# Kernel optimization log

Measured on AMD Instinct MI355X. Metric: run time of the kernel, lower is better.

The kernel has to match this reference:

```python
import jax, jax.numpy as jnp
import numpy as np

L_S = 4  # segment length (== factor in __init__)


def dtw_dist(x, y):
    """Exact 1-D DTW distance with |a-b| cost (the quantity fastdtw approximates).

    Row recurrence d[i,j] = C[i,j] + min(d[i-1,j], d[i-1,j-1], d[i,j-1]) is
    solved per row in closed form: with a[j]=min(prev[j],prev[j-1]),
    b[j]=C[i,j]+a[j], S=cumsum(C[i]), we have d[i,:] = S + cummin(b - S).
    """
    C = jnp.abs(x[:, None] - y[None, :])  # [n, m] cost matrix
    big = jnp.asarray(jnp.finfo(C.dtype).max, C.dtype)
    row0 = jnp.cumsum(C[0])  # first DP row: cumulative cost

    def step(prev, c):
        shifted = jnp.concatenate([jnp.full((1,), big, prev.dtype), prev[:-1]])
        a = jnp.minimum(prev, shifted)          # min(d[i-1,j], d[i-1,j-1])
        S = jnp.cumsum(c)
        d = S + jax.lax.cummin(a + c - S)       # min-plus prefix scan
        return d, None

    last, _ = jax.lax.scan(step, row0, C[1:])
    return last[-1]


def setup_inputs() -> dict:
    key = jax.random.key(0)
    kq, kk, kv = jax.random.split(key, 3)
    B, L, H, D = 1, 32, 8, 32
    return {
        "queries": jax.random.normal(kq, (B, L, H, D), dtype=jnp.float32),
        "keys": jax.random.normal(kk, (B, L, H, D), dtype=jnp.float32),
        "values": jax.random.normal(kv, (B, L, H, D), dtype=jnp.float32),
        "attn_mask": jnp.zeros((1,), dtype=bool),  # unused, as in original
    }


def reference(queries, keys, values, attn_mask):
    B, Lq, H, D = queries.shape
    Lk = keys.shape[1]
    Ls = L_S
    scale = 1.0 / np.sqrt(Ls).astype(np.float32)
    Nq, Nk = Lq // Ls, Lk // Ls  # L divisible by Ls -> no addition_Q path

    seg_q = queries.reshape(B, Nq, Ls, H, D)
    seg_k = keys.reshape(B, Nk, Ls, H, D)
    seg_v = values.reshape(B, Nk, Ls, H, D)

    # Original flattens each segment over (B, Ls, H, D) before fastdtw, so the
    # distance is identical for every (b, h): a single [Nq, Nk] matrix.
    flat_q = jnp.moveaxis(seg_q, 1, 0).reshape(Nq, -1)  # [Nq, B*Ls*H*D]
    flat_k = jnp.moveaxis(seg_k, 1, 0).reshape(Nk, -1)  # [Nk, B*Ls*H*D]

    dists = jax.vmap(lambda xq: jax.vmap(lambda xk: dtw_dist(xq, xk))(flat_k))(flat_q)  # [Nq, Nk]

    A = jax.nn.softmax(scale * dists, axis=-1)  # [Nq, Nk], broadcast over (B, H)

    # Softmax-weighted sum of value segments (intended semantics of the
    # expanded matmul): V[b,i,t,h,d] = sum_j A[i,j] * seg_v[b,j,t,h,d]
    V = jnp.einsum('ij,bjthd->bithd', A, seg_v).reshape(B, Nq * Ls, H, D)
    return V
```

## Files before the change

### kernel.cpp

```cpp
#include <hip/hip_runtime.h>
#include <float.h>

#define NSEG 8
#define SEGLEN 1024
#define BIGV 1e30f
#define PADV 1e18f

#define NW 4
#define CH 64
#define NCH 17
#define XLEN 1152
#define BSTRIDE 1160

#define DPPF(OLD, SRC, CTRL, RM, BM, BC)                                      \
    __int_as_float(__builtin_amdgcn_update_dpp(                               \
        __float_as_int(OLD), __float_as_int(SRC), CTRL, RM, BM, BC))
#define WSHIFT1(OLD, SRC) DPPF(OLD, SRC, 0x138, 0xF, 0xF, false)

__device__ __forceinline__ float readlaneF(float v, int l) {
    return __int_as_float(__builtin_amdgcn_readlane(__float_as_int(v), l));
}

__global__ __launch_bounds__(256) void dtw_sk4_kernel(const float* __restrict__ q,
                                                      const float* __restrict__ kk,
                                                      float* __restrict__ dists) {
    __shared__ float xl[XLEN];
    __shared__ float bnd[NW + 1][BSTRIDE];
    __shared__ float dump[128];
    __shared__ int flagsA[NW + 1];
    const int tid = threadIdx.x;
    const int lane = tid & 63;
    const int wv = tid >> 6;
    const int pair = blockIdx.x;
    const float* __restrict__ x = q + (pair >> 3) * SEGLEN;
    const float* __restrict__ y = kk + (pair & 7) * SEGLEN;

    for (int t = tid; t < XLEN; t += 256) xl[t] = (t < SEGLEN) ? x[t] : PADV;
    for (int t = tid; t < (NW + 1) * BSTRIDE; t += 256)
        (&bnd[0][0])[t] = (t == 63) ? 0.f : BIGV;
    if (tid < NW + 1) flagsA[tid] = (tid == 0) ? 0x7FFFFFFF : 0;

    const float4 y4 = *(const float4*)(y + wv * 256 + lane * 4);
    const float yv0 = y4.x, yv1 = y4.y, yv2 = y4.z, yv3 = y4.w;

    __syncthreads();

    const float* __restrict__ br = &bnd[wv][0];

    {
        const int need0 = (NCH < 2) ? NCH : 2;
        while (__hip_atomic_load(&flagsA[wv], __ATOMIC_ACQUIRE,
                                 __HIP_MEMORY_SCOPE_WORKGROUP) < need0)
            __builtin_amdgcn_s_sleep(1);
    }
    float P0 = BIGV, P1 = BIGV, P2 = BIGV, P3 = BIGV, xreg = PADV;
    float lf = br[64];
    float dgl = br[63];

#define STEP(s) {                                                             \
    xreg = WSHIFT1(readlaneF(xv, (s)), xreg);                                 \
    const float c0n = fabsf(xreg - yv0) + fminf(fminf(P0, lf), dgl);          \
    const float c1n = fabsf(xreg - yv1) + fminf(fminf(P1, c0n), P0);          \
    const float c2n = fabsf(xreg - yv2) + fminf(fminf(P2, c1n), P1);          \
    const float c3n = fabsf(xreg - yv3) + fminf(fminf(P3, c2n), P2);          \
    const float n1 = WSHIFT1(readlaneF(bvv, (s)), c3n);                       \
    dgl = lf; lf = n1; P0 = c0n; P1 = c1n; P2 = c2n; P3 = c3n;                \
    va[(s)] = c3n;                                                            \
}
#define STEP8(s) STEP(s) STEP((s)+1) STEP((s)+2) STEP((s)+3)                  \
                 STEP((s)+4) STEP((s)+5) STEP((s)+6) STEP((s)+7)

#pragma unroll 1
    for (int tc = 0; tc < NCH; ++tc) {
        const int need = (tc + 2 < NCH) ? (tc + 2) : NCH;
        while (__hip_atomic_load(&flagsA[wv], __ATOMIC_ACQUIRE,
                                 __HIP_MEMORY_SCOPE_WORKGROUP) < need)
            __builtin_amdgcn_s_sleep(1);

        const float xv = xl[CH * tc + lane];
        const float bvv = br[CH * tc + 65 + lane];
        float* va = (lane == 63) ? &bnd[wv + 1][CH * tc + 1] : &dump[lane];

        STEP8(0) STEP8(8) STEP8(16) STEP8(24) STEP8(32) STEP8(40) STEP8(48) STEP8(56)

        __hip_atomic_store(&flagsA[wv + 1], tc + 1, __ATOMIC_RELEASE,
                           __HIP_MEMORY_SCOPE_WORKGROUP);
    }
#undef STEP
#undef STEP8

    if (wv == NW - 1 && lane == 0) dists[pair] = bnd[NW][1087];
}

__global__ __launch_bounds__(256) void softmax_out_kernel(const float* __restrict__ v,
                                                          const float* __restrict__ dists,
                                                          float* __restrict__ out) {
    const int o = blockIdx.x * blockDim.x + threadIdx.x;
    if (o >= NSEG * SEGLEN) return;
    const int i = o >> 10;
    const int p = o & 1023;

    float l[NSEG];
    float mx = -FLT_MAX;
#pragma unroll
    for (int j = 0; j < NSEG; ++j) {
        l[j] = 0.5f * dists[i * NSEG + j];
        mx = fmaxf(mx, l[j]);
    }
    float s = 0.f;
#pragma unroll
    for (int j = 0; j < NSEG; ++j) {
        l[j] = expf(l[j] - mx);
        s += l[j];
    }
    const float inv = 1.f / s;
    float acc = 0.f;
#pragma unroll
    for (int j = 0; j < NSEG; ++j) acc += (l[j] * inv) * v[j * SEGLEN + p];
    out[o] = acc;
}

extern "C" void kernel_launch(void* const* d_in, const int* in_sizes, int n_in,
                              void* d_out, int out_size, void* d_ws, size_t ws_size,
                              hipStream_t stream) {
    const float* q = (const float*)d_in[0];
    const float* k = (const float*)d_in[1];
    const float* v = (const float*)d_in[2];
    float* out = (float*)d_out;
    float* dists = (float*)d_ws;

    dtw_sk4_kernel<<<dim3(NSEG * NSEG), dim3(256), 0, stream>>>(q, k, dists);
    softmax_out_kernel<<<dim3((NSEG * SEGLEN + 255) / 256), dim3(256), 0, stream>>>(v, dists, out);
}
```

Baseline: 66.36 us.

## Replace readlane broadcasts with DPP row-shift streams and min-plus prefix form

Each step used to broadcast lane s with v_readlane, going through a scalar register, before shifting it into the wavefront. The inputs are now kept in registers that rotate each step with a DPP wave-shift-left, so lane 0 always holds the next element and no scalar round trip is needed. The four-column recurrence per lane is also rewritten into the closed form cumsum-plus-prefix-min, which shortens the serial dependency chain across columns at the cost of a few extra adds and subtracts. This can change floating-point rounding slightly, and it depends on the DPP 0x130 control code performing a whole-wave shift.

```diff
diff --git a/kernel.cpp b/kernel.cpp
--- a/kernel.cpp
+++ b/kernel.cpp
@@ -16,10 +16,7 @@
     __int_as_float(__builtin_amdgcn_update_dpp(                               \
         __float_as_int(OLD), __float_as_int(SRC), CTRL, RM, BM, BC))
 #define WSHIFT1(OLD, SRC) DPPF(OLD, SRC, 0x138, 0xF, 0xF, false)
-
-__device__ __forceinline__ float readlaneF(float v, int l) {
-    return __int_as_float(__builtin_amdgcn_readlane(__float_as_int(v), l));
-}
+#define WSTREAM(SRC) DPPF(SRC, SRC, 0x130, 0xF, 0xF, false)
 
 __global__ __launch_bounds__(256) void dtw_sk4_kernel(const float* __restrict__ q,
                                                       const float* __restrict__ kk,
@@ -58,14 +55,25 @@
     float dgl = br[63];
 
 #define STEP(s) {                                                             \
-    xreg = WSHIFT1(readlaneF(xv, (s)), xreg);                                 \
-    const float c0n = fabsf(xreg - yv0) + fminf(fminf(P0, lf), dgl);          \
-    const float c1n = fabsf(xreg - yv1) + fminf(fminf(P1, c0n), P0);          \
-    const float c2n = fabsf(xreg - yv2) + fminf(fminf(P2, c1n), P1);          \
-    const float c3n = fabsf(xreg - yv3) + fminf(fminf(P3, c2n), P2);          \
-    const float n1 = WSHIFT1(readlaneF(bvv, (s)), c3n);                       \
-    dgl = lf; lf = n1; P0 = c0n; P1 = c1n; P2 = c2n; P3 = c3n;                \
-    va[(s)] = c3n;                                                            \
+    xreg = WSHIFT1(xstr, xreg);                                               \
+    xstr = WSTREAM(xstr);                                                     \
+    const float ls0 = fabsf(xreg - yv0);                                      \
+    const float ls1 = ls0 + fabsf(xreg - yv1);                                \
+    const float ls2 = ls1 + fabsf(xreg - yv2);                                \
+    const float ls3 = ls2 + fabsf(xreg - yv3);                                \
+    const float a0 = fminf(P0, dgl);                                          \
+    const float a1 = fminf(P1, P0);                                           \
+    const float a2 = fminf(P2, P1);                                           \
+    const float a3 = fminf(P3, P2);                                           \
+    const float r0 = fminf(a0, lf);                                           \
+    const float r1 = fminf(r0, a1 - ls0);                                     \
+    const float r2 = fminf(r1, a2 - ls1);                                     \
+    const float r3 = fminf(r2, a3 - ls2);                                     \
+    P0 = ls0 + r0; P1 = ls1 + r1; P2 = ls2 + r2; P3 = ls3 + r3;               \
+    const float n1 = WSHIFT1(bstr, P3);                                       \
+    bstr = WSTREAM(bstr);                                                     \
+    dgl = lf; lf = n1;                                                        \
+    va[(s)] = P3;                                                             \
 }
 #define STEP8(s) STEP(s) STEP((s)+1) STEP((s)+2) STEP((s)+3)                  \
                  STEP((s)+4) STEP((s)+5) STEP((s)+6) STEP((s)+7)
@@ -77,8 +85,8 @@
                                  __HIP_MEMORY_SCOPE_WORKGROUP) < need)
             __builtin_amdgcn_s_sleep(1);
 
-        const float xv = xl[CH * tc + lane];
-        const float bvv = br[CH * tc + 65 + lane];
+        float xstr = xl[CH * tc + lane];
+        float bstr = br[CH * tc + 65 + lane];
         float* va = (lane == 63) ? &bnd[wv + 1][CH * tc + 1] : &dump[lane];
 
         STEP8(0) STEP8(8) STEP8(16) STEP8(24) STEP8(32) STEP8(40) STEP8(48) STEP8(56)
```

Result: slower. 85.87 us (+29.4%).

## Process two DTW rows per wavefront step to halve skewed wavefront steps

Applied to the files above, without the earlier changes.

Each lane now advances two DP rows (even and odd) per DPP shift step instead of one, so a 64-row chunk needs 32 lane-shift steps and the skewed pipeline fill shrinks from one row per lane to two rows per lane. Boundary stores become float2 writes and the chunk count and boundary offsets change to match the new skew. The aim is to cut the wavefront diagonal latency and per-row DPP/readlane overhead. In exchange each step has a longer serial dependency chain and higher register pressure, and the inter-wave dependency is relaxed to three chunks ahead.

```diff
diff --git a/kernel.cpp b/kernel.cpp
--- a/kernel.cpp
+++ b/kernel.cpp
@@ -7,10 +7,11 @@
 #define PADV 1e18f
 
 #define NW 4
-#define CH 64
-#define NCH 17
+#define CHD 32
+#define NCHD 18
 #define XLEN 1152
-#define BSTRIDE 1160
+#define BOFF 128
+#define BSTRIDE 1288
 
 #define DPPF(OLD, SRC, CTRL, RM, BM, BC)                                      \
     __int_as_float(__builtin_amdgcn_update_dpp(                               \
@@ -21,12 +22,12 @@
     return __int_as_float(__builtin_amdgcn_readlane(__float_as_int(v), l));
 }
 
-__global__ __launch_bounds__(256) void dtw_sk4_kernel(const float* __restrict__ q,
+__global__ __launch_bounds__(256) void dtw_rs2_kernel(const float* __restrict__ q,
                                                       const float* __restrict__ kk,
                                                       float* __restrict__ dists) {
     __shared__ float xl[XLEN];
     __shared__ float bnd[NW + 1][BSTRIDE];
-    __shared__ float dump[128];
+    __shared__ float2 dumpf2[96];
     __shared__ int flagsA[NW + 1];
     const int tid = threadIdx.x;
     const int lane = tid & 63;
@@ -37,7 +38,7 @@
 
     for (int t = tid; t < XLEN; t += 256) xl[t] = (t < SEGLEN) ? x[t] : PADV;
     for (int t = tid; t < (NW + 1) * BSTRIDE; t += 256)
-        (&bnd[0][0])[t] = (t == 63) ? 0.f : BIGV;
+        (&bnd[0][0])[t] = (t == BOFF - 1) ? 0.f : BIGV;
     if (tid < NW + 1) flagsA[tid] = (tid == 0) ? 0x7FFFFFFF : 0;
 
     const float4 y4 = *(const float4*)(y + wv * 256 + lane * 4);
@@ -48,48 +49,69 @@
     const float* __restrict__ br = &bnd[wv][0];
 
     {
-        const int need0 = (NCH < 2) ? NCH : 2;
+        const int need0 = (NCHD < 2) ? NCHD : 2;
         while (__hip_atomic_load(&flagsA[wv], __ATOMIC_ACQUIRE,
                                  __HIP_MEMORY_SCOPE_WORKGROUP) < need0)
             __builtin_amdgcn_s_sleep(1);
     }
-    float P0 = BIGV, P1 = BIGV, P2 = BIGV, P3 = BIGV, xreg = PADV;
-    float lf = br[64];
-    float dgl = br[63];
+    float Q0 = BIGV, Q1 = BIGV, Q2 = BIGV, Q3 = BIGV;
+    float xe = PADV, xo = PADV;
+    float lfe = br[BOFF];
+    float lfo = br[BOFF + 1];
+    float dgl = br[BOFF - 1];
 
-#define STEP(s) {                                                             \
-    xreg = WSHIFT1(readlaneF(xv, (s)), xreg);                                 \
-    const float c0n = fabsf(xreg - yv0) + fminf(fminf(P0, lf), dgl);          \
-    const float c1n = fabsf(xreg - yv1) + fminf(fminf(P1, c0n), P0);          \
-    const float c2n = fabsf(xreg - yv2) + fminf(fminf(P2, c1n), P1);          \
-    const float c3n = fabsf(xreg - yv3) + fminf(fminf(P3, c2n), P2);          \
-    const float n1 = WSHIFT1(readlaneF(bvv, (s)), c3n);                       \
-    dgl = lf; lf = n1; P0 = c0n; P1 = c1n; P2 = c2n; P3 = c3n;                \
-    va[(s)] = c3n;                                                            \
+#define DSTEP(s, xpe, xpo, bpe, bpo) {                                        \
+    xe = WSHIFT1(xpe, xe);                                                    \
+    xo = WSHIFT1(xpo, xo);                                                    \
+    const float ce0 = fabsf(xe - yv0) + fminf(fminf(Q0, lfe), dgl);           \
+    const float ce1 = fabsf(xe - yv1) + fminf(fminf(Q1, ce0), Q0);            \
+    const float ce2 = fabsf(xe - yv2) + fminf(fminf(Q2, ce1), Q1);            \
+    const float ce3 = fabsf(xe - yv3) + fminf(fminf(Q3, ce2), Q2);            \
+    const float co0 = fabsf(xo - yv0) + fminf(fminf(ce0, lfo), lfe);          \
+    const float co1 = fabsf(xo - yv1) + fminf(fminf(ce1, co0), ce0);          \
+    const float co2 = fabsf(xo - yv2) + fminf(fminf(ce2, co1), ce1);          \
+    const float co3 = fabsf(xo - yv3) + fminf(fminf(ce3, co2), ce2);          \
+    const float n1e = WSHIFT1(bpe, ce3);                                      \
+    const float n1o = WSHIFT1(bpo, co3);                                      \
+    dgl = lfo; lfe = n1e; lfo = n1o;                                          \
+    Q0 = co0; Q1 = co1; Q2 = co2; Q3 = co3;                                   \
+    va[(s)] = make_float2(ce3, co3);                                          \
 }
-#define STEP8(s) STEP(s) STEP((s)+1) STEP((s)+2) STEP((s)+3)                  \
-                 STEP((s)+4) STEP((s)+5) STEP((s)+6) STEP((s)+7)
+#define DSTEP4(s) {                                                           \
+    const float xe0 = readlaneF(xv, 2*(s)+0), xo0 = readlaneF(xv, 2*(s)+1);   \
+    const float xe1 = readlaneF(xv, 2*(s)+2), xo1 = readlaneF(xv, 2*(s)+3);   \
+    const float xe2 = readlaneF(xv, 2*(s)+4), xo2 = readlaneF(xv, 2*(s)+5);   \
+    const float xe3 = readlaneF(xv, 2*(s)+6), xo3 = readlaneF(xv, 2*(s)+7);   \
+    const float be0 = readlaneF(bv, 2*(s)+0), bo0 = readlaneF(bv, 2*(s)+1);   \
+    const float be1 = readlaneF(bv, 2*(s)+2), bo1 = readlaneF(bv, 2*(s)+3);   \
+    const float be2 = readlaneF(bv, 2*(s)+4), bo2 = readlaneF(bv, 2*(s)+5);   \
+    const float be3 = readlaneF(bv, 2*(s)+6), bo3 = readlaneF(bv, 2*(s)+7);   \
+    DSTEP((s)+0, xe0, xo0, be0, bo0) DSTEP((s)+1, xe1, xo1, be1, bo1)         \
+    DSTEP((s)+2, xe2, xo2, be2, bo2) DSTEP((s)+3, xe3, xo3, be3, bo3)         \
+}
 
 #pragma unroll 1
-    for (int tc = 0; tc < NCH; ++tc) {
-        const int need = (tc + 2 < NCH) ? (tc + 2) : NCH;
+    for (int tc = 0; tc < NCHD; ++tc) {
+        const int need = (tc + 3 < NCHD) ? (tc + 3) : NCHD;
         while (__hip_atomic_load(&flagsA[wv], __ATOMIC_ACQUIRE,
                                  __HIP_MEMORY_SCOPE_WORKGROUP) < need)
             __builtin_amdgcn_s_sleep(1);
 
-        const float xv = xl[CH * tc + lane];
-        const float bvv = br[CH * tc + 65 + lane];
-        float* va = (lane == 63) ? &bnd[wv + 1][CH * tc + 1] : &dump[lane];
+        const float xv = xl[64 * tc + lane];
+        const float bv = br[64 * tc + BOFF + 2 + lane];
+        float2* va = (lane == 63) ? (float2*)&bnd[wv + 1][64 * tc + 2]
+                                  : dumpf2 + lane;
 
-        STEP8(0) STEP8(8) STEP8(16) STEP8(24) STEP8(32) STEP8(40) STEP8(48) STEP8(56)
+        DSTEP4(0)  DSTEP4(4)  DSTEP4(8)  DSTEP4(12)
+        DSTEP4(16) DSTEP4(20) DSTEP4(24) DSTEP4(28)
 
         __hip_atomic_store(&flagsA[wv + 1], tc + 1, __ATOMIC_RELEASE,
                            __HIP_MEMORY_SCOPE_WORKGROUP);
     }
-#undef STEP
-#undef STEP8
+#undef DSTEP
+#undef DSTEP4
 
-    if (wv == NW - 1 && lane == 0) dists[pair] = bnd[NW][1087];
+    if (wv == NW - 1 && lane == 0) dists[pair] = bnd[NW][1151];
 }
 
 __global__ __launch_bounds__(256) void softmax_out_kernel(const float* __restrict__ v,
@@ -129,6 +151,6 @@
     float* out = (float*)d_out;
     float* dists = (float*)d_ws;
 
-    dtw_sk4_kernel<<<dim3(NSEG * NSEG), dim3(256), 0, stream>>>(q, k, dists);
+    dtw_rs2_kernel<<<dim3(NSEG * NSEG), dim3(256), 0, stream>>>(q, k, dists);
     softmax_out_kernel<<<dim3((NSEG * SEGLEN + 255) / 256), dim3(256), 0, stream>>>(v, dists, out);
 }
```

Result: slower. 70.78 us (+6.7%).
